# Performance work log

Hardware: AMD Instinct MI355X
Metric: run time of the kernel (lower is better)

The kernel has to match this reference:

```python
import jax, jax.numpy as jnp
import numpy as np

RES, IN, OUT = 1024, 16, 8
LEAK = 0.7
SPECTRAL_RADIUS = 0.9
CONNECTIVITY = 0.1


def _init_reservoir(rng):
    W = rng.standard_normal((RES, RES)).astype(np.float32)
    mask = rng.random((RES, RES)) > CONNECTIVITY
    W[mask] = 0.0
    sr = np.max(np.abs(np.linalg.eigvals(W)))
    return (W * (SPECTRAL_RADIUS / sr)).astype(np.float32)


def setup_inputs() -> dict:
    key = jax.random.key(0)
    k1, k2, k3, k4 = jax.random.split(key, 4)
    rng = np.random.default_rng(0)
    B, S = 32, 4096
    x = jax.random.normal(k1, (B, S, IN), dtype=jnp.float32)
    state = jnp.zeros((B, RES), dtype=jnp.float32)
    W_in = jax.random.normal(k2, (RES, IN), dtype=jnp.float32)
    W_res = jnp.asarray(_init_reservoir(rng))
    lim = 1.0 / np.sqrt(RES)
    W_out_w = jax.random.uniform(k3, (OUT, RES), minval=-lim, maxval=lim, dtype=jnp.float32)
    W_out_b = jax.random.uniform(k4, (OUT,), minval=-lim, maxval=lim, dtype=jnp.float32)
    return {"x": x, "state": state, "W_in": W_in, "W_res": W_res,
            "W_out_w": W_out_w, "W_out_b": W_out_b}


def reference(x, state, W_in, W_res, W_out_w, W_out_b):
    # Precompute input projections for all steps: [B, S, RES]
    inp = jnp.einsum('bsi,ri->bsr', x, W_in)

    def step(h, u_t):
        # u_t: [B, RES] precomputed input term at time t
        new_h = (1.0 - LEAK) * h + LEAK * jnp.tanh(u_t + h @ W_res.T)
        return new_h, new_h

    # scan over time axis
    final_state, states = jax.lax.scan(step, state, jnp.swapaxes(inp, 0, 1))
    states = jnp.swapaxes(states, 0, 1)  # [B, S, RES]
    outputs = jnp.einsum('bsr,or->bso', states, W_out_w) + W_out_b
    return outputs, final_state
```

## Files before the change

### kernel.cpp

```cpp
#include <hip/hip_runtime.h>
#include <stdint.h>

#define RES     1024
#define INPD    16
#define OUTD    8
#define BATCH   32
#define SEQ     4096
#define NCMAX   24
#define PASSPAD 3
#define GROUP   4
#define NBLK    (BATCH * GROUP)
#define KMAX    6

#define MAT_BYTES ((size_t)NCMAX * RES * 8 * 4)

__global__ __launch_bounds__(32) void esn_count(const float* __restrict__ W,
                                                uint32_t* __restrict__ eff) {
  const int r = blockIdx.x, b = threadIdx.x;
  const float* row = W + (size_t)r * RES;
  int n = 0;
  for (int k = 0; k < 32; ++k) n += (row[b + 32 * k] != 0.0f) ? 1 : 0;
  int t3 = (n > PASSPAD) ? (n - PASSPAD) : 0;
  for (int o = 16; o; o >>= 1) t3 += __shfl_down(t3, o, 32);
  if (b == 0) eff[r] = (uint32_t)(PASSPAD * 32 + t3);
}

__global__ __launch_bounds__(1024) void esn_sort(const uint32_t* __restrict__ eff,
                                                 uint32_t* __restrict__ perm,
                                                 uint32_t* __restrict__ wnc) {
  __shared__ uint32_t key[RES];
  const int tid = threadIdx.x;
  key[tid] = (eff[tid] << 10) | (uint32_t)tid;
  __syncthreads();
  for (int len = 2; len <= RES; len <<= 1) {
    for (int s = len >> 1; s > 0; s >>= 1) {
      const int j = tid ^ s;
      if (j > tid) {
        const uint32_t a = key[tid], c = key[j];
        const bool up = ((tid & len) == 0);
        if ((a > c) == up) { key[tid] = c; key[j] = a; }
      }
      __syncthreads();
    }
  }
  const uint32_t k = key[tid];
  perm[tid] = k & 1023u;
  if ((tid & 63) == 63) {
    uint32_t c = ((k >> 10) + 7u) >> 3;
    wnc[tid >> 6] = (c < (uint32_t)NCMAX) ? c : (uint32_t)NCMAX;
  }
}

__global__ __launch_bounds__(32) void esn_pack(const float* __restrict__ W,
                                               const uint32_t* __restrict__ perm,
                                               uint32_t* __restrict__ mato) {
  const int p = blockIdx.x;
  const int b = threadIdx.x;
  __shared__ float    vls[32][16];
  __shared__ uint16_t cls[32][16];
  __shared__ int      cnt[32];
  __shared__ uint32_t rr;
  if (b == 0) rr = perm[p];
  __syncthreads();
  const float* row = W + (size_t)rr * RES;

  int n = 0;
  for (int k = 0; k < 32; ++k) {
    const float v = row[b + 32 * k];
    if (v != 0.0f && n < 16) { vls[b][n] = v; cls[b][n] = (uint16_t)(b + 32 * k); ++n; }
  }
  cnt[b] = n;
  const int rot = p & 31;
  for (int e = b; e < NCMAX * 8; e += 32) {
    const uint32_t padcol = (uint32_t)((rot + (e & 31)) & 31);
    mato[(size_t)(e >> 3) * (RES * 8) + (size_t)p * 8 + (e & 7)] = padcol << 18;
  }
  __syncthreads();

  const int myord = (b - rot) & 31;
  for (int k2 = 0; k2 < n; ++k2) {
    int rank;
    if (k2 < PASSPAD) {
      rank = k2 * 32 + myord;
    } else {
      rank = PASSPAD * 32;
      const int kp = k2 - PASSPAD;
      for (int b2 = 0; b2 < 32; ++b2) {
        int cp = cnt[b2] - PASSPAD; cp = (cp > 0) ? cp : 0;
        const int ord = (b2 - rot) & 31;
        const int lim = kp + ((ord < myord) ? 1 : 0);
        rank += (cp < lim) ? cp : lim;
      }
    }
    if (rank < NCMAX * 8) {
      const uint32_t u  = __float_as_uint(vls[b][k2]);
      const uint32_t bf = (u + 0x7FFFu + ((u >> 16) & 1u)) >> 16;
      mato[(size_t)(rank >> 3) * (RES * 8) + (size_t)p * 8 + (rank & 7)] =
          ((uint32_t)cls[b][k2] << 18) | bf;
    }
  }
}

__global__ void esn_init(uint32_t* __restrict__ cnt) {
  if (threadIdx.x < NBLK) cnt[threadIdx.x] = 0;
}

#define GATHER8(QA, QB)                                                       \
  a0 = fmaf(__uint_as_float((QA).x << 16), hc[(QA).x >> 18], a0);             \
  a1 = fmaf(__uint_as_float((QA).y << 16), hc[(QA).y >> 18], a1);             \
  a2 = fmaf(__uint_as_float((QA).z << 16), hc[(QA).z >> 18], a2);             \
  a3 = fmaf(__uint_as_float((QA).w << 16), hc[(QA).w >> 18], a3);             \
  a0 = fmaf(__uint_as_float((QB).x << 16), hc[(QB).x >> 18], a0);             \
  a1 = fmaf(__uint_as_float((QB).y << 16), hc[(QB).y >> 18], a1);             \
  a2 = fmaf(__uint_as_float((QB).z << 16), hc[(QB).z >> 18], a2);             \
  a3 = fmaf(__uint_as_float((QB).w << 16), hc[(QB).w >> 18], a3);

__global__ __launch_bounds__(1024) void esn_scan(
    const float* __restrict__ x, const float* __restrict__ state,
    const float* __restrict__ Win, const float* __restrict__ Woutw,
    const float* __restrict__ Woutb,
    const uint32_t* __restrict__ mat, const uint32_t* __restrict__ perm,
    const uint32_t* __restrict__ wnc,
    uint32_t* __restrict__ cnt, float* __restrict__ pub,
    float* __restrict__ out) {
  __shared__ float hbuf[2][RES];
  __shared__ float4 xbuf[2][INPD / 4];
  __shared__ __align__(16) float psum[256][4];
  __shared__ uint32_t perml[RES];

  const int bid  = blockIdx.x;
  const int grp  = bid >> 2;
  const int role = bid & 3;
  const int tid  = threadIdx.x;
  const int l    = tid & 63;
  const int v    = tid >> 6;
  const int seg  = v >> 2;
  const int lw   = v & 3;
  const int W    = lw * 4 + role;
  const int p    = W * 64 + l;
  const int row  = (int)perm[p];
  const int ncw  = ((int)__builtin_amdgcn_readfirstlane(wnc[W]) + 3 - seg) >> 2;

  perml[tid] = perm[tid];

  const float4 w4 = ((const float4*)(Win + (size_t)row * INPD))[seg];

  float wo[16];
  const float* wor = Woutw + (size_t)v * RES;
#pragma unroll
  for (int j = 0; j < 16; ++j) wo[j] = (v < OUTD) ? wor[l + 64 * j] : 0.0f;
  const float bw = (v < OUTD) ? Woutb[v] : 0.0f;

  uint4 qa[KMAX], qb[KMAX];
#pragma unroll
  for (int k = 0; k < KMAX; ++k) {
    if (k < ncw) {
      const uint32_t* cp = mat + (size_t)(seg + 4 * k) * (RES * 8) + (size_t)p * 8;
      qa[k] = *(const uint4*)cp;
      qb[k] = *(const uint4*)(cp + 4);
    } else {
      qa[k] = make_uint4(0, 0, 0, 0);
      qb[k] = make_uint4(0, 0, 0, 0);
    }
  }

  hbuf[0][tid] = state[(size_t)grp * RES + tid];
  float hreg = (tid < 256) ? state[(size_t)grp * RES + row] : 0.0f;
  const float* xr = x + (size_t)grp * SEQ * INPD;
  if (tid < INPD / 4) xbuf[0][tid] = ((const float4*)xr)[tid];
  __syncthreads();

  for (int t = 0; t < SEQ; ++t) {
    const int par = t & 1;
    const float* hc = hbuf[par];

    if (t > 0 && role == ((t - 1) & 3) && v < OUTD) {
      float s = 0.0f;
#pragma unroll
      for (int j = 0; j < 16; ++j) s = fmaf(hc[l + 64 * j], wo[j], s);
#pragma unroll
      for (int d = 1; d < 64; d <<= 1) s += __shfl_xor(s, d);
      if (l == 0) out[((size_t)grp * SEQ + (t - 1)) * OUTD + v] = s + bw;
    }
    if (v == 15 && l < INPD / 4 && t + 1 < SEQ)
      xbuf[par ^ 1][l] = ((const float4*)(xr + (size_t)(t + 1) * INPD))[l];

    const float4 xv = xbuf[par][seg];
    float a0 = 0.f, a1 = 0.f, a2 = 0.f, a3 = 0.f;
    a0 = fmaf(xv.x, w4.x, a0); a1 = fmaf(xv.y, w4.y, a1);
    a2 = fmaf(xv.z, w4.z, a2); a3 = fmaf(xv.w, w4.w, a3);
#pragma unroll
    for (int k = 0; k < KMAX; ++k) {
      if (k < ncw) { GATHER8(qa[k], qb[k]) }
    }
    psum[lw * 64 + l][seg] = (a0 + a1) + (a2 + a3);
    __syncthreads();

    float* ppub = pub + ((size_t)(par ^ 1) * BATCH + grp) * RES;
    if (tid < 256) {
      const float4 ps = *(const float4*)&psum[tid][0];
      const float acc = (ps.x + ps.y) + (ps.z + ps.w);
      const float e  = exp2f(acc * 2.885390081777927f);
      const float th = 1.0f - 2.0f * __builtin_amdgcn_rcpf(e + 1.0f);
      const float hn = fmaf(0.7f, th, 0.3f * hreg);
      hreg = hn;
      hbuf[par ^ 1][row] = hn;
      __hip_atomic_store(&ppub[p], hn, __ATOMIC_RELAXED,
                         __HIP_MEMORY_SCOPE_AGENT);
    }
    __syncthreads();

    if (tid == 0)
      __hip_atomic_store(&cnt[bid], (uint32_t)(t + 1), __ATOMIC_RELEASE,
                         __HIP_MEMORY_SCOPE_AGENT);
    if (tid < GROUP && tid != role) {
      const uint32_t want = (uint32_t)(t + 1);
      while (__hip_atomic_load(&cnt[grp * GROUP + tid], __ATOMIC_ACQUIRE,
                               __HIP_MEMORY_SCOPE_AGENT) < want)
        __builtin_amdgcn_s_sleep(2);
    }
    __syncthreads();

    if (v >= 4) {
      const int j  = v - 4;
      const int gg = j / 3, m = j - gg * 3;
      const int ro = m + ((m >= role) ? 1 : 0);
      const int pp = (gg * 4 + ro) * 64 + l;
      const float hv = __hip_atomic_load(&ppub[pp], __ATOMIC_RELAXED,
                                         __HIP_MEMORY_SCOPE_AGENT);
      hbuf[par ^ 1][perml[pp]] = hv;
    }
    __syncthreads();
  }

  if (role == 0) {
    if (v < OUTD) {
      float s = 0.0f;
#pragma unroll
      for (int j = 0; j < 16; ++j) s = fmaf(hbuf[0][l + 64 * j], wo[j], s);
#pragma unroll
      for (int d = 1; d < 64; d <<= 1) s += __shfl_xor(s, d);
      if (l == 0) out[((size_t)grp * SEQ + (SEQ - 1)) * OUTD + v] = s + bw;
    }
    float* finals = out + (size_t)BATCH * SEQ * OUTD;
    finals[(size_t)grp * RES + tid] = hbuf[0][tid];
  }
}

extern "C" void kernel_launch(void* const* d_in, const int* in_sizes, int n_in,
                              void* d_out, int out_size, void* d_ws, size_t ws_size,
                              hipStream_t stream) {
  const float* x     = (const float*)d_in[0];
  const float* state = (const float*)d_in[1];
  const float* Win   = (const float*)d_in[2];
  const float* Wres  = (const float*)d_in[3];
  const float* Woutw = (const float*)d_in[4];
  const float* Woutb = (const float*)d_in[5];
  float* out = (float*)d_out;

  uint8_t*  ws   = (uint8_t*)d_ws;
  uint32_t* mat  = (uint32_t*)ws;
  uint32_t* eff  = (uint32_t*)(ws + MAT_BYTES);
  uint32_t* perm = (uint32_t*)(ws + MAT_BYTES + 4096);
  uint32_t* wnc  = (uint32_t*)(ws + MAT_BYTES + 8192);
  uint32_t* cnt  = (uint32_t*)(ws + MAT_BYTES + 12288);
  float*    pub  = (float*)(ws + MAT_BYTES + 16384);

  esn_count<<<RES, 32, 0, stream>>>(Wres, eff);
  esn_sort<<<1, RES, 0, stream>>>(eff, perm, wnc);
  esn_pack<<<RES, 32, 0, stream>>>(Wres, perm, mat);
  esn_init<<<1, 128, 0, stream>>>(cnt);
  esn_scan<<<NBLK, RES, 0, stream>>>(x, state, Win, Woutw, Woutb,
                                     mat, perm, wnc, cnt, pub, out);
}
```

Measured before the change: 20.30 ms.

## Split each reservoir across 8 blocks and interleave two batch rows to hide sync latency

Each group of blocks now handles two batch elements instead of one, and each element's 1024 rows are split across 8 cooperating blocks instead of 4. The two elements' recurrent steps are interleaved, so the cross-block wait for one element's published state overlaps with computing the other element. Each thread now holds fewer sparse weight chunks. The cost is more blocks sharing each state exchange, so more global publish and poll traffic per step and a more complex two-counter protocol.

```diff
diff --git a/kernel.cpp b/kernel.cpp
--- a/kernel.cpp
+++ b/kernel.cpp
@@ -8,11 +8,13 @@
 #define SEQ     4096
 #define NCMAX   24
 #define PASSPAD 3
-#define GROUP   4
-#define NBLK    (BATCH * GROUP)
-#define KMAX    6
+#define GROUP   8
+#define NPAIR   16
+#define NBLK    (NPAIR * GROUP)
+#define KMAX    3
 
 #define MAT_BYTES ((size_t)NCMAX * RES * 8 * 4)
+#define PUBOFF(par, bs, g) ((((size_t)(par) * 2 + (bs)) * NPAIR + (g)) * RES)
 
 __global__ __launch_bounds__(32) void esn_count(const float* __restrict__ W,
                                                 uint32_t* __restrict__ eff) {
@@ -101,8 +103,8 @@
   }
 }
 
-__global__ void esn_init(uint32_t* __restrict__ cnt) {
-  if (threadIdx.x < NBLK) cnt[threadIdx.x] = 0;
+__global__ void esn_init(uint32_t* __restrict__ cntA, uint32_t* __restrict__ cntB) {
+  if (threadIdx.x < NBLK) { cntA[threadIdx.x] = 0; cntB[threadIdx.x] = 0; }
 }
 
 #define GATHER8(QA, QB)                                                       \
@@ -121,29 +123,31 @@
     const float* __restrict__ Woutb,
     const uint32_t* __restrict__ mat, const uint32_t* __restrict__ perm,
     const uint32_t* __restrict__ wnc,
-    uint32_t* __restrict__ cnt, float* __restrict__ pub,
-    float* __restrict__ out) {
-  __shared__ float hbuf[2][RES];
-  __shared__ float4 xbuf[2][INPD / 4];
-  __shared__ __align__(16) float psum[256][4];
+    uint32_t* __restrict__ cntA, uint32_t* __restrict__ cntB,
+    float* __restrict__ pub, float* __restrict__ out) {
+  __shared__ float hbufA[2][RES], hbufB[2][RES];
+  __shared__ float psum[8][128];
   __shared__ uint32_t perml[RES];
+  __shared__ __align__(16) float xA[2][INPD], xB[2][INPD];
 
   const int bid  = blockIdx.x;
-  const int grp  = bid >> 2;
-  const int role = bid & 3;
+  const int grp  = bid >> 3;
+  const int role = bid & 7;
+  const int gA   = grp * 2, gB = grp * 2 + 1;
   const int tid  = threadIdx.x;
   const int l    = tid & 63;
   const int v    = tid >> 6;
-  const int seg  = v >> 2;
-  const int lw   = v & 3;
-  const int W    = lw * 4 + role;
-  const int p    = W * 64 + l;
+  const int sw   = (v & 1) ? (15 - role) : role;
+  const int seg  = v >> 1;
+  const int p    = sw * 64 + l;
   const int row  = (int)perm[p];
-  const int ncw  = ((int)__builtin_amdgcn_readfirstlane(wnc[W]) + 3 - seg) >> 2;
+  const int wncv = (int)__builtin_amdgcn_readfirstlane(wnc[sw]);
+  const int nct  = (wncv - seg + 7) >> 3;
 
   perml[tid] = perm[tid];
 
-  const float4 w4 = ((const float4*)(Win + (size_t)row * INPD))[seg];
+  const float wi0 = Win[(size_t)row * INPD + 2 * seg];
+  const float wi1 = Win[(size_t)row * INPD + 2 * seg + 1];
 
   float wo[16];
   const float* wor = Woutw + (size_t)v * RES;
@@ -153,97 +157,179 @@
 
   uint4 qa[KMAX], qb[KMAX];
 #pragma unroll
-  for (int k = 0; k < KMAX; ++k) {
-    if (k < ncw) {
-      const uint32_t* cp = mat + (size_t)(seg + 4 * k) * (RES * 8) + (size_t)p * 8;
-      qa[k] = *(const uint4*)cp;
-      qb[k] = *(const uint4*)(cp + 4);
+  for (int kk = 0; kk < KMAX; ++kk) {
+    if (kk < nct) {
+      const uint32_t* cp = mat + ((size_t)(seg + 8 * kk) * RES + (size_t)p) * 8;
+      qa[kk] = *(const uint4*)cp;
+      qb[kk] = *(const uint4*)(cp + 4);
     } else {
-      qa[k] = make_uint4(0, 0, 0, 0);
-      qb[k] = make_uint4(0, 0, 0, 0);
-    }
-  }
-
-  hbuf[0][tid] = state[(size_t)grp * RES + tid];
-  float hreg = (tid < 256) ? state[(size_t)grp * RES + row] : 0.0f;
-  const float* xr = x + (size_t)grp * SEQ * INPD;
-  if (tid < INPD / 4) xbuf[0][tid] = ((const float4*)xr)[tid];
-  __syncthreads();
-
-  for (int t = 0; t < SEQ; ++t) {
-    const int par = t & 1;
-    const float* hc = hbuf[par];
-
-    if (t > 0 && role == ((t - 1) & 3) && v < OUTD) {
+      qa[kk] = make_uint4(0, 0, 0, 0);
+      qb[kk] = make_uint4(0, 0, 0, 0);
+    }
+  }
+
+  hbufA[0][tid] = state[(size_t)gA * RES + tid];
+  hbufB[0][tid] = state[(size_t)gB * RES + tid];
+  float hregA = (tid < 128) ? state[(size_t)gA * RES + row] : 0.0f;
+  float hregB = (tid < 128) ? state[(size_t)gB * RES + row] : 0.0f;
+  const float* xrA = x + (size_t)gA * SEQ * INPD;
+  const float* xrB = x + (size_t)gB * SEQ * INPD;
+  if (v == 15 && l < INPD / 4) ((float4*)xA[0])[l] = ((const float4*)xrA)[l];
+  if (v == 14 && l < INPD / 4) ((float4*)xB[0])[l] = ((const float4*)xrB)[l];
+  __syncthreads();
+
+  int cp_pos = 0, cp_row = 0;
+  if (v >= 2) {
+    const int j  = v - 2;
+    int t1 = j + ((j >= role) ? 1 : 0);
+    t1 += ((t1 >= 15 - role) ? 1 : 0);
+    cp_pos = t1 * 64 + l;
+    cp_row = (int)perml[cp_pos];
+  }
+  float* finals = out + (size_t)BATCH * SEQ * OUTD;
+
+  for (int k = 0; k < SEQ; ++k) {
+    const int par = k & 1;
+
+    if (v == 15 && l < INPD / 4 && k + 1 < SEQ)
+      ((float4*)xA[par ^ 1])[l] = ((const float4*)(xrA + (size_t)(k + 1) * INPD))[l];
+    if (k > 0 && role == ((k - 1) & 7) && v < OUTD) {
+      const float* hc = hbufA[par];
       float s = 0.0f;
 #pragma unroll
       for (int j = 0; j < 16; ++j) s = fmaf(hc[l + 64 * j], wo[j], s);
 #pragma unroll
       for (int d = 1; d < 64; d <<= 1) s += __shfl_xor(s, d);
-      if (l == 0) out[((size_t)grp * SEQ + (t - 1)) * OUTD + v] = s + bw;
-    }
-    if (v == 15 && l < INPD / 4 && t + 1 < SEQ)
-      xbuf[par ^ 1][l] = ((const float4*)(xr + (size_t)(t + 1) * INPD))[l];
-
-    const float4 xv = xbuf[par][seg];
-    float a0 = 0.f, a1 = 0.f, a2 = 0.f, a3 = 0.f;
-    a0 = fmaf(xv.x, w4.x, a0); a1 = fmaf(xv.y, w4.y, a1);
-    a2 = fmaf(xv.z, w4.z, a2); a3 = fmaf(xv.w, w4.w, a3);
-#pragma unroll
-    for (int k = 0; k < KMAX; ++k) {
-      if (k < ncw) { GATHER8(qa[k], qb[k]) }
-    }
-    psum[lw * 64 + l][seg] = (a0 + a1) + (a2 + a3);
-    __syncthreads();
-
-    float* ppub = pub + ((size_t)(par ^ 1) * BATCH + grp) * RES;
-    if (tid < 256) {
-      const float4 ps = *(const float4*)&psum[tid][0];
-      const float acc = (ps.x + ps.y) + (ps.z + ps.w);
-      const float e  = exp2f(acc * 2.885390081777927f);
+      if (l == 0) out[((size_t)gA * SEQ + (k - 1)) * OUTD + v] = s + bw;
+    }
+    {
+      const float* hc = hbufA[par];
+      float a0 = wi0 * xA[par][2 * seg], a1 = wi1 * xA[par][2 * seg + 1];
+      float a2 = 0.0f, a3 = 0.0f;
+#pragma unroll
+      for (int kk = 0; kk < KMAX; ++kk) {
+        if (kk < nct) { GATHER8(qa[kk], qb[kk]) }
+      }
+      psum[seg][(v & 1) * 64 + l] = (a0 + a1) + (a2 + a3);
+    }
+    __syncthreads();
+    if (tid < 128) {
+      float s = 0.0f;
+#pragma unroll
+      for (int s8 = 0; s8 < 8; ++s8) s += psum[s8][tid];
+      const float e  = exp2f(s * 2.885390081777927f);
       const float th = 1.0f - 2.0f * __builtin_amdgcn_rcpf(e + 1.0f);
-      const float hn = fmaf(0.7f, th, 0.3f * hreg);
-      hreg = hn;
-      hbuf[par ^ 1][row] = hn;
-      __hip_atomic_store(&ppub[p], hn, __ATOMIC_RELAXED,
+      const float hn = fmaf(0.7f, th, 0.3f * hregA);
+      hregA = hn;
+      hbufA[par ^ 1][row] = hn;
+      __hip_atomic_store(&pub[PUBOFF(par ^ 1, 0, grp) + p], hn,
+                         __ATOMIC_RELAXED, __HIP_MEMORY_SCOPE_AGENT);
+    }
+    __syncthreads();
+    if (tid == 0)
+      __hip_atomic_store(&cntA[bid], (uint32_t)(k + 1), __ATOMIC_RELEASE,
                          __HIP_MEMORY_SCOPE_AGENT);
-    }
-    __syncthreads();
-
+
+    if (k > 0) {
+      if (tid < GROUP && tid != role) {
+        const uint32_t want = (uint32_t)k;
+        while (__hip_atomic_load(&cntB[grp * GROUP + tid], __ATOMIC_ACQUIRE,
+                                 __HIP_MEMORY_SCOPE_AGENT) < want)
+          __builtin_amdgcn_s_sleep(1);
+      }
+      __syncthreads();
+      if (v >= 2)
+        hbufB[par][cp_row] =
+            __hip_atomic_load(&pub[PUBOFF(par, 1, grp) + cp_pos],
+                              __ATOMIC_RELAXED, __HIP_MEMORY_SCOPE_AGENT);
+    }
+    __syncthreads();
+
+    if (v == 14 && l < INPD / 4 && k + 1 < SEQ)
+      ((float4*)xB[par ^ 1])[l] = ((const float4*)(xrB + (size_t)(k + 1) * INPD))[l];
+    if (k > 0 && role == ((k - 1) & 7) && v < OUTD) {
+      const float* hc = hbufB[par];
+      float s = 0.0f;
+#pragma unroll
+      for (int j = 0; j < 16; ++j) s = fmaf(hc[l + 64 * j], wo[j], s);
+#pragma unroll
+      for (int d = 1; d < 64; d <<= 1) s += __shfl_xor(s, d);
+      if (l == 0) out[((size_t)gB * SEQ + (k - 1)) * OUTD + v] = s + bw;
+    }
+    {
+      const float* hc = hbufB[par];
+      float a0 = wi0 * xB[par][2 * seg], a1 = wi1 * xB[par][2 * seg + 1];
+      float a2 = 0.0f, a3 = 0.0f;
+#pragma unroll
+      for (int kk = 0; kk < KMAX; ++kk) {
+        if (kk < nct) { GATHER8(qa[kk], qb[kk]) }
+      }
+      psum[seg][(v & 1) * 64 + l] = (a0 + a1) + (a2 + a3);
+    }
+    __syncthreads();
+    if (tid < 128) {
+      float s = 0.0f;
+#pragma unroll
+      for (int s8 = 0; s8 < 8; ++s8) s += psum[s8][tid];
+      const float e  = exp2f(s * 2.885390081777927f);
+      const float th = 1.0f - 2.0f * __builtin_amdgcn_rcpf(e + 1.0f);
+      const float hn = fmaf(0.7f, th, 0.3f * hregB);
+      hregB = hn;
+      hbufB[par ^ 1][row] = hn;
+      __hip_atomic_store(&pub[PUBOFF(par ^ 1, 1, grp) + p], hn,
+                         __ATOMIC_RELAXED, __HIP_MEMORY_SCOPE_AGENT);
+    }
+    __syncthreads();
     if (tid == 0)
-      __hip_atomic_store(&cnt[bid], (uint32_t)(t + 1), __ATOMIC_RELEASE,
+      __hip_atomic_store(&cntB[bid], (uint32_t)(k + 1), __ATOMIC_RELEASE,
                          __HIP_MEMORY_SCOPE_AGENT);
+
     if (tid < GROUP && tid != role) {
-      const uint32_t want = (uint32_t)(t + 1);
-      while (__hip_atomic_load(&cnt[grp * GROUP + tid], __ATOMIC_ACQUIRE,
+      const uint32_t want = (uint32_t)(k + 1);
+      while (__hip_atomic_load(&cntA[grp * GROUP + tid], __ATOMIC_ACQUIRE,
                                __HIP_MEMORY_SCOPE_AGENT) < want)
-        __builtin_amdgcn_s_sleep(2);
-    }
-    __syncthreads();
-
-    if (v >= 4) {
-      const int j  = v - 4;
-      const int gg = j / 3, m = j - gg * 3;
-      const int ro = m + ((m >= role) ? 1 : 0);
-      const int pp = (gg * 4 + ro) * 64 + l;
-      const float hv = __hip_atomic_load(&ppub[pp], __ATOMIC_RELAXED,
-                                         __HIP_MEMORY_SCOPE_AGENT);
-      hbuf[par ^ 1][perml[pp]] = hv;
-    }
-    __syncthreads();
-  }
+        __builtin_amdgcn_s_sleep(1);
+    }
+    __syncthreads();
+    if (v >= 2)
+      hbufA[par ^ 1][cp_row] =
+          __hip_atomic_load(&pub[PUBOFF(par ^ 1, 0, grp) + cp_pos],
+                            __ATOMIC_RELAXED, __HIP_MEMORY_SCOPE_AGENT);
+    __syncthreads();
+  }
+
+  if (tid < GROUP && tid != role) {
+    while (__hip_atomic_load(&cntB[grp * GROUP + tid], __ATOMIC_ACQUIRE,
+                             __HIP_MEMORY_SCOPE_AGENT) < (uint32_t)SEQ)
+      __builtin_amdgcn_s_sleep(1);
+  }
+  __syncthreads();
+  if (v >= 2)
+    hbufB[0][cp_row] =
+        __hip_atomic_load(&pub[PUBOFF(0, 1, grp) + cp_pos],
+                          __ATOMIC_RELAXED, __HIP_MEMORY_SCOPE_AGENT);
+  __syncthreads();
 
   if (role == 0) {
     if (v < OUTD) {
-      float s = 0.0f;
-#pragma unroll
-      for (int j = 0; j < 16; ++j) s = fmaf(hbuf[0][l + 64 * j], wo[j], s);
-#pragma unroll
-      for (int d = 1; d < 64; d <<= 1) s += __shfl_xor(s, d);
-      if (l == 0) out[((size_t)grp * SEQ + (SEQ - 1)) * OUTD + v] = s + bw;
-    }
-    float* finals = out + (size_t)BATCH * SEQ * OUTD;
-    finals[(size_t)grp * RES + tid] = hbuf[0][tid];
+      float sA = 0.0f, sB = 0.0f;
+#pragma unroll
+      for (int j = 0; j < 16; ++j) {
+        sA = fmaf(hbufA[0][l + 64 * j], wo[j], sA);
+        sB = fmaf(hbufB[0][l + 64 * j], wo[j], sB);
+      }
+#pragma unroll
+      for (int d = 1; d < 64; d <<= 1) {
+        sA += __shfl_xor(sA, d);
+        sB += __shfl_xor(sB, d);
+      }
+      if (l == 0) {
+        out[((size_t)gA * SEQ + (SEQ - 1)) * OUTD + v] = sA + bw;
+        out[((size_t)gB * SEQ + (SEQ - 1)) * OUTD + v] = sB + bw;
+      }
+    }
+    finals[(size_t)gA * RES + tid] = hbufA[0][tid];
+    finals[(size_t)gB * RES + tid] = hbufB[0][tid];
   }
 }
 
@@ -263,13 +349,14 @@
   uint32_t* eff  = (uint32_t*)(ws + MAT_BYTES);
   uint32_t* perm = (uint32_t*)(ws + MAT_BYTES + 4096);
   uint32_t* wnc  = (uint32_t*)(ws + MAT_BYTES + 8192);
-  uint32_t* cnt  = (uint32_t*)(ws + MAT_BYTES + 12288);
+  uint32_t* cntA = (uint32_t*)(ws + MAT_BYTES + 12288);
+  uint32_t* cntB = (uint32_t*)(ws + MAT_BYTES + 14336);
   float*    pub  = (float*)(ws + MAT_BYTES + 16384);
 
   esn_count<<<RES, 32, 0, stream>>>(Wres, eff);
   esn_sort<<<1, RES, 0, stream>>>(eff, perm, wnc);
   esn_pack<<<RES, 32, 0, stream>>>(Wres, perm, mat);
-  esn_init<<<1, 128, 0, stream>>>(cnt);
+  esn_init<<<1, 256, 0, stream>>>(cntA, cntB);
   esn_scan<<<NBLK, RES, 0, stream>>>(x, state, Win, Woutw, Woutb,
-                                     mat, perm, wnc, cnt, pub, out);
-}
+                                     mat, perm, wnc, cntA, cntB, pub, out);
+}
```

Measured after the change: 26.86 ms. 32.3% more time.
